# Optimization experiments

Hardware: AMD Instinct MI355X
Metric: run time of the kernel (lower is better)

The kernel has to match this reference:

```python
import jax, jax.numpy as jnp
import numpy as np

N = 200000
HID = 256
HEADS = 8
HD = HID // HEADS
C = 1000  # num clusters


def setup_inputs() -> dict:
    key = jax.random.key(0)
    ks = jax.random.split(key, 8)
    s = 1.0 / np.sqrt(HID)
    return {
        "x": jax.random.normal(ks[0], (N, HID), dtype=jnp.float32),
        "cluster_assignments": jax.random.randint(ks[1], (N,), 0, C),
        "batch": jnp.zeros((N,), dtype=jnp.int64),
        "Wk": jax.random.uniform(ks[2], (HID, HID), minval=-s, maxval=s),
        "bk": jnp.zeros((HID,), dtype=jnp.float32),
        "Wv": jax.random.uniform(ks[3], (HID, HID), minval=-s, maxval=s),
        "bv": jnp.zeros((HID,), dtype=jnp.float32),
        "Wo": jax.random.uniform(ks[4], (HID, HID), minval=-s, maxval=s),
        "bo": jnp.zeros((HID,), dtype=jnp.float32),
        "pool_query": jax.random.normal(ks[5], (1, HEADS, HD), dtype=jnp.float32),
    }


def reference(x, cluster_assignments, batch, Wk, bk, Wv, bv, Wo, bo, pool_query):
    seg = cluster_assignments
    scale = HD ** -0.5
    keys = (x @ Wk.T + bk).reshape(-1, HEADS, HD)     # [N, H, D]
    values = (x @ Wv.T + bv).reshape(-1, HEADS, HD)   # [N, H, D]
    # attention scores per node/head against shared pool query
    scores = jnp.einsum('nhd,hd->nh', keys, pool_query[0]) * scale  # [N, H]
    # segment-wise (per-cluster) softmax over nodes, per head
    m = jax.ops.segment_max(scores, seg, num_segments=C)            # [C, H]
    e = jnp.exp(scores - m[seg])                                    # [N, H]
    z = jax.ops.segment_sum(e, seg, num_segments=C)                 # [C, H]
    w = e / z[seg]                                                  # [N, H]
    attended = (w[..., None] * values).reshape(-1, HID)             # [N, HID]
    # scatter_mean over clusters
    ssum = jax.ops.segment_sum(attended, seg, num_segments=C)       # [C, HID]
    cnt = jax.ops.segment_sum(jnp.ones((attended.shape[0],), attended.dtype), seg, num_segments=C)
    pooled = ssum / jnp.clip(cnt, 1.0)[:, None]                     # [C, HID]
    out = pooled @ Wo.T + bo                                        # [C, HID]
    return out[seg]                                                 # [N, HID]
```

## Files before the change

kernel.cpp:

```cpp
#include <hip/hip_runtime.h>
#include <math.h>

#define HID 256
#define HEADS 8
#define HD 32
#define C_CLUST 1000
#define SCALEQ 0.17677669529663687f
#define CAP 512

__device__ inline unsigned enc_m(float f) {
  unsigned b = __float_as_uint(f);
  unsigned mask = (b & 0x80000000u) ? 0xFFFFFFFFu : 0x80000000u;
  return b ^ mask;
}
__device__ inline float dec_m(unsigned u) {
  unsigned b = (u & 0x80000000u) ? (u ^ 0x80000000u) : ~u;
  return __uint_as_float(b);
}

__global__ __launch_bounds__(256) void k_prep(const float* __restrict__ Wk,
                                              const float* __restrict__ bk,
                                              const float* __restrict__ pq,
                                              float* __restrict__ qk,
                                              float* __restrict__ cb,
                                              int* __restrict__ cur,
                                              unsigned* __restrict__ mtab) {
  __shared__ float qv[HD];
  int h = blockIdx.x;
  int t = threadIdx.x;
  int g = h * 256 + t;
  for (int i = g; i < C_CLUST; i += 2048) cur[i] = 0;
  for (int i = g; i < C_CLUST * 8; i += 2048) mtab[i] = 0u;
  if (t < HD) qv[t] = pq[h * HD + t];
  __syncthreads();
  float a = 0.f;
#pragma unroll 8
  for (int d = 0; d < HD; ++d) a += Wk[(size_t)(h * HD + d) * HID + t] * qv[d];
  qk[h * HID + t] = a * SCALEQ;
  if (t == 0) {
    float s = 0.f;
    for (int d = 0; d < HD; ++d) s += bk[h * HD + d] * qv[d];
    cb[h] = s * SCALEQ;
  }
}

__global__ __launch_bounds__(256) void k_scores(const float* __restrict__ x,
                                                const int* __restrict__ seg,
                                                const float* __restrict__ qk,
                                                const float* __restrict__ cb,
                                                float* __restrict__ scores,
                                                int* __restrict__ cur,
                                                unsigned* __restrict__ mtab,
                                                int* __restrict__ list, int N) {
  int lane = threadIdx.x & 63;
  int wid = (int)(((size_t)blockIdx.x * blockDim.x + threadIdx.x) >> 6);
  int nw = (int)(((size_t)gridDim.x * blockDim.x) >> 6);
  float4 q4[8];
#pragma unroll
  for (int h = 0; h < 8; ++h) q4[h] = *(const float4*)(qk + h * HID + 4 * lane);
  float cbv = cb[lane & 7];
  for (int n = wid; n < N; n += nw) {
    float4 xv = *(const float4*)(x + (size_t)n * HID + 4 * lane);
    float r0 = xv.x * q4[0].x + xv.y * q4[0].y + xv.z * q4[0].z + xv.w * q4[0].w;
    float r1 = xv.x * q4[1].x + xv.y * q4[1].y + xv.z * q4[1].z + xv.w * q4[1].w;
    float r2 = xv.x * q4[2].x + xv.y * q4[2].y + xv.z * q4[2].z + xv.w * q4[2].w;
    float r3 = xv.x * q4[3].x + xv.y * q4[3].y + xv.z * q4[3].z + xv.w * q4[3].w;
    float r4 = xv.x * q4[4].x + xv.y * q4[4].y + xv.z * q4[4].z + xv.w * q4[4].w;
    float r5 = xv.x * q4[5].x + xv.y * q4[5].y + xv.z * q4[5].z + xv.w * q4[5].w;
    float r6 = xv.x * q4[6].x + xv.y * q4[6].y + xv.z * q4[6].z + xv.w * q4[6].w;
    float r7 = xv.x * q4[7].x + xv.y * q4[7].y + xv.z * q4[7].z + xv.w * q4[7].w;
    r0 += __shfl_xor(r0, 1); r0 += __shfl_xor(r0, 2); r0 += __shfl_xor(r0, 4);
    r1 += __shfl_xor(r1, 1); r1 += __shfl_xor(r1, 2); r1 += __shfl_xor(r1, 4);
    r2 += __shfl_xor(r2, 1); r2 += __shfl_xor(r2, 2); r2 += __shfl_xor(r2, 4);
    r3 += __shfl_xor(r3, 1); r3 += __shfl_xor(r3, 2); r3 += __shfl_xor(r3, 4);
    r4 += __shfl_xor(r4, 1); r4 += __shfl_xor(r4, 2); r4 += __shfl_xor(r4, 4);
    r5 += __shfl_xor(r5, 1); r5 += __shfl_xor(r5, 2); r5 += __shfl_xor(r5, 4);
    r6 += __shfl_xor(r6, 1); r6 += __shfl_xor(r6, 2); r6 += __shfl_xor(r6, 4);
    r7 += __shfl_xor(r7, 1); r7 += __shfl_xor(r7, 2); r7 += __shfl_xor(r7, 4);
    int p = lane & 7;
    float v = (p < 4) ? ((p < 2) ? (p == 0 ? r0 : r1) : (p == 2 ? r2 : r3))
                      : ((p < 6) ? (p == 4 ? r4 : r5) : (p == 6 ? r6 : r7));
    v += __shfl_xor(v, 8); v += __shfl_xor(v, 16); v += __shfl_xor(v, 32);
    v += cbv;
    if (lane < 8) {
      int c = seg[n];
      scores[(size_t)n * 8 + lane] = v;
      atomicMax(&mtab[c * 8 + lane], enc_m(v));
      if (lane == 0) {
        int pos = atomicAdd(&cur[c], 1);
        if (pos < CAP) list[c * CAP + pos] = n;
      }
    }
  }
}

__global__ __launch_bounds__(256) void k_pool(const float* __restrict__ x,
                                              const float* __restrict__ scores,
                                              const unsigned* __restrict__ mtab,
                                              const int* __restrict__ cur,
                                              const int* __restrict__ list,
                                              const float* __restrict__ Wv,
                                              const float* __restrict__ bv,
                                              const float* __restrict__ Wo,
                                              const float* __restrict__ bo,
                                              float* __restrict__ outc) {
  __shared__ float e_lds[CAP][8];
  __shared__ float s_lds[8 * HID];
  __shared__ float red[256];
  __shared__ float p_lds[HID];
  int c = blockIdx.x;
  int t = threadIdx.x;
  int cnt = cur[c];
  if (cnt == 0) return;
  int cntL = (cnt < CAP) ? cnt : CAP;

  int h8 = t & 7;
  int i0 = t >> 3;
  int rq = t >> 6, cl = t & 63;
  float mh = dec_m(mtab[c * 8 + h8]);
  const int* lp = list + c * CAP;

  float pz = 0.f;
  for (int i = i0; i < cntL; i += 32) {
    float ev = __expf(scores[(size_t)lp[i] * 8 + h8] - mh);
    e_lds[i][h8] = ev;
    pz += ev;
  }
  red[t] = pz;
  __syncthreads();

  float4 acc[8];
#pragma unroll
  for (int h = 0; h < 8; ++h) acc[h] = make_float4(0.f, 0.f, 0.f, 0.f);
  int i = rq;
  for (; i + 12 < cntL; i += 16) {
    int n0 = lp[i], n1 = lp[i + 4], n2 = lp[i + 8], n3 = lp[i + 12];
    float4 x0 = *(const float4*)(x + (size_t)n0 * HID + 4 * cl);
    float4 x1 = *(const float4*)(x + (size_t)n1 * HID + 4 * cl);
    float4 x2 = *(const float4*)(x + (size_t)n2 * HID + 4 * cl);
    float4 x3 = *(const float4*)(x + (size_t)n3 * HID + 4 * cl);
    float4 ea, eb;
#define ACC8(XV, ROW)                                                        \
    ea = *(const float4*)&e_lds[ROW][0]; eb = *(const float4*)&e_lds[ROW][4]; \
    { float eh[8] = {ea.x, ea.y, ea.z, ea.w, eb.x, eb.y, eb.z, eb.w};         \
      _Pragma("unroll")                                                       \
      for (int h = 0; h < 8; ++h) {                                           \
        acc[h].x += eh[h] * XV.x; acc[h].y += eh[h] * XV.y;                   \
        acc[h].z += eh[h] * XV.z; acc[h].w += eh[h] * XV.w; } }
    ACC8(x0, i)
    ACC8(x1, i + 4)
    ACC8(x2, i + 8)
    ACC8(x3, i + 12)
  }
  for (; i < cntL; i += 4) {
    int n0 = lp[i];
    float4 x0 = *(const float4*)(x + (size_t)n0 * HID + 4 * cl);
    float4 ea, eb;
    ACC8(x0, i)
  }
#undef ACC8

  for (int s = 128; s >= 8; s >>= 1) {
    __syncthreads();
    if (t < s) red[t] += red[t + s];
  }
  __syncthreads();
  float zinv[8];
#pragma unroll
  for (int h = 0; h < 8; ++h) {
    float z = red[h];
    zinv[h] = (z > 0.f) ? 1.f / z : 0.f;
  }

  float4* buf = (float4*)e_lds;
#pragma unroll
  for (int h = 0; h < 8; ++h) {
    __syncthreads();
    buf[t] = acc[h];
    __syncthreads();
    if (t < 64) {
      float4 a = buf[t], b = buf[t + 64], c4 = buf[t + 128], d4 = buf[t + 192];
      float sc = zinv[h];
      float4 r;
      r.x = (a.x + b.x + c4.x + d4.x) * sc;
      r.y = (a.y + b.y + c4.y + d4.y) * sc;
      r.z = (a.z + b.z + c4.z + d4.z) * sc;
      r.w = (a.w + b.w + c4.w + d4.w) * sc;
      *(float4*)&s_lds[h * HID + 4 * t] = r;
    }
  }
  __syncthreads();

  int grp = t >> 2, q = t & 3;
  float rc = 1.f / (float)cnt;
#pragma unroll
  for (int r = 0; r < 4; ++r) {
    int o = grp + 64 * r;
    const float4* wr = (const float4*)(Wv + (size_t)o * HID);
    const float4* sr = (const float4*)(s_lds + (o >> 5) * HID);
    float a = 0.f;
#pragma unroll
    for (int k = 0; k < 16; ++k) {
      float4 w4 = wr[q + 4 * k];
      float4 s4 = sr[q + 4 * k];
      a += w4.x * s4.x + w4.y * s4.y + w4.z * s4.z + w4.w * s4.w;
    }
    a += __shfl_xor(a, 1);
    a += __shfl_xor(a, 2);
    if (q == 0) p_lds[o] = (a + bv[o]) * rc;
  }
  __syncthreads();
#pragma unroll
  for (int r = 0; r < 4; ++r) {
    int o = grp + 64 * r;
    const float4* wr = (const float4*)(Wo + (size_t)o * HID);
    const float4* pr = (const float4*)p_lds;
    float a = 0.f;
#pragma unroll
    for (int k = 0; k < 16; ++k) {
      float4 w4 = wr[q + 4 * k];
      float4 p4 = pr[q + 4 * k];
      a += w4.x * p4.x + w4.y * p4.y + w4.z * p4.z + w4.w * p4.w;
    }
    a += __shfl_xor(a, 1);
    a += __shfl_xor(a, 2);
    if (q == 0) outc[(size_t)c * HID + o] = a + bo[o];
  }
}

__global__ __launch_bounds__(256) void k_expand(const int* __restrict__ seg,
                                                const float* __restrict__ out_c,
                                                float* __restrict__ out, int N) {
  size_t g = (size_t)blockIdx.x * blockDim.x + threadIdx.x;
  size_t total = (size_t)N * (HID / 4);
  size_t stride = (size_t)gridDim.x * blockDim.x;
  const float4* oc = (const float4*)out_c;
  float4* o4 = (float4*)out;
  for (; g < total; g += stride) {
    int n = (int)(g >> 6);
    int q = (int)(g & 63);
    int c = seg[n];
    o4[g] = oc[(size_t)c * 64 + q];
  }
}

extern "C" void kernel_launch(void* const* d_in, const int* in_sizes, int n_in,
                              void* d_out, int out_size, void* d_ws, size_t ws_size,
                              hipStream_t stream) {
  const float* x = (const float*)d_in[0];
  const int* seg = (const int*)d_in[1];
  const float* Wk = (const float*)d_in[3];
  const float* bk = (const float*)d_in[4];
  const float* Wv = (const float*)d_in[5];
  const float* bv = (const float*)d_in[6];
  const float* Wo = (const float*)d_in[7];
  const float* bo = (const float*)d_in[8];
  const float* pq = (const float*)d_in[9];
  int N = in_sizes[0] / HID;

  char* ws = (char*)d_ws;
  size_t cur_off = 0;
  auto take = [&](size_t bytes) -> void* {
    void* p = ws + cur_off;
    cur_off += (bytes + 255) & ~(size_t)255;
    return p;
  };
  float* qk = (float*)take((size_t)HEADS * HID * 4);
  float* cb = (float*)take((size_t)HEADS * 4);
  int* cur = (int*)take((size_t)C_CLUST * 4);
  unsigned* mtab = (unsigned*)take((size_t)C_CLUST * 8 * 4);
  int* list = (int*)take((size_t)C_CLUST * CAP * 4);
  float* scr = (float*)take((size_t)N * 8 * 4);
  float* outc = (float*)take((size_t)C_CLUST * HID * 4);

  k_prep<<<HEADS, 256, 0, stream>>>(Wk, bk, pq, qk, cb, cur, mtab);
  int sb = (N + 31) / 32;
  k_scores<<<sb, 256, 0, stream>>>(x, seg, qk, cb, scr, cur, mtab, list, N);
  k_pool<<<C_CLUST, 256, 0, stream>>>(x, scr, mtab, cur, list, Wv, bv, Wo, bo, outc);
  k_expand<<<2048, 256, 0, stream>>>(seg, outc, (float*)d_out, N);
}
```

Measured before the change: 190.1 us.

## Fuse cluster-output expansion into pool kernel and deepen gather unroll

New measurement: 180.2 us. 1.05x faster.

```diff
diff --git a/kernel.cpp b/kernel.cpp
--- a/kernel.cpp
+++ b/kernel.cpp
@@ -7,6 +7,8 @@
 #define C_CLUST 1000
 #define SCALEQ 0.17677669529663687f
 #define CAP 512
+
+typedef float fx4 __attribute__((ext_vector_type(4)));
 
 __device__ inline unsigned enc_m(float f) {
   unsigned b = __float_as_uint(f);
@@ -103,11 +105,12 @@
                                               const float* __restrict__ bv,
                                               const float* __restrict__ Wo,
                                               const float* __restrict__ bo,
-                                              float* __restrict__ outc) {
+                                              float* __restrict__ out) {
   __shared__ float e_lds[CAP][8];
   __shared__ float s_lds[8 * HID];
   __shared__ float red[256];
   __shared__ float p_lds[HID];
+  __shared__ float orow[HID];
   int c = blockIdx.x;
   int t = threadIdx.x;
   int cnt = cur[c];
@@ -132,30 +135,33 @@
   float4 acc[8];
 #pragma unroll
   for (int h = 0; h < 8; ++h) acc[h] = make_float4(0.f, 0.f, 0.f, 0.f);
+  const float* xb = x + 4 * cl;
+#define ACC8(XV, ROW)                                                          \
+  { float4 ea = *(const float4*)&e_lds[ROW][0];                                \
+    float4 eb = *(const float4*)&e_lds[ROW][4];                                \
+    float eh[8] = {ea.x, ea.y, ea.z, ea.w, eb.x, eb.y, eb.z, eb.w};            \
+    _Pragma("unroll")                                                          \
+    for (int h = 0; h < 8; ++h) {                                              \
+      acc[h].x += eh[h] * XV.x; acc[h].y += eh[h] * XV.y;                      \
+      acc[h].z += eh[h] * XV.z; acc[h].w += eh[h] * XV.w; } }
   int i = rq;
-  for (; i + 12 < cntL; i += 16) {
-    int n0 = lp[i], n1 = lp[i + 4], n2 = lp[i + 8], n3 = lp[i + 12];
-    float4 x0 = *(const float4*)(x + (size_t)n0 * HID + 4 * cl);
-    float4 x1 = *(const float4*)(x + (size_t)n1 * HID + 4 * cl);
-    float4 x2 = *(const float4*)(x + (size_t)n2 * HID + 4 * cl);
-    float4 x3 = *(const float4*)(x + (size_t)n3 * HID + 4 * cl);
-    float4 ea, eb;
-#define ACC8(XV, ROW)                                                        \
-    ea = *(const float4*)&e_lds[ROW][0]; eb = *(const float4*)&e_lds[ROW][4]; \
-    { float eh[8] = {ea.x, ea.y, ea.z, ea.w, eb.x, eb.y, eb.z, eb.w};         \
-      _Pragma("unroll")                                                       \
-      for (int h = 0; h < 8; ++h) {                                           \
-        acc[h].x += eh[h] * XV.x; acc[h].y += eh[h] * XV.y;                   \
-        acc[h].z += eh[h] * XV.z; acc[h].w += eh[h] * XV.w; } }
-    ACC8(x0, i)
-    ACC8(x1, i + 4)
-    ACC8(x2, i + 8)
-    ACC8(x3, i + 12)
+  for (; i + 28 < cntL; i += 32) {
+    int n0 = lp[i +  0], n1 = lp[i +  4], n2 = lp[i +  8], n3 = lp[i + 12];
+    int n4 = lp[i + 16], n5 = lp[i + 20], n6 = lp[i + 24], n7 = lp[i + 28];
+    float4 x0 = *(const float4*)(xb + (size_t)n0 * HID);
+    float4 x1 = *(const float4*)(xb + (size_t)n1 * HID);
+    float4 x2 = *(const float4*)(xb + (size_t)n2 * HID);
+    float4 x3 = *(const float4*)(xb + (size_t)n3 * HID);
+    float4 x4 = *(const float4*)(xb + (size_t)n4 * HID);
+    float4 x5 = *(const float4*)(xb + (size_t)n5 * HID);
+    float4 x6 = *(const float4*)(xb + (size_t)n6 * HID);
+    float4 x7 = *(const float4*)(xb + (size_t)n7 * HID);
+    ACC8(x0, i +  0) ACC8(x1, i +  4) ACC8(x2, i +  8) ACC8(x3, i + 12)
+    ACC8(x4, i + 16) ACC8(x5, i + 20) ACC8(x6, i + 24) ACC8(x7, i + 28)
   }
   for (; i < cntL; i += 4) {
     int n0 = lp[i];
-    float4 x0 = *(const float4*)(x + (size_t)n0 * HID + 4 * cl);
-    float4 ea, eb;
+    float4 x0 = *(const float4*)(xb + (size_t)n0 * HID);
     ACC8(x0, i)
   }
 #undef ACC8
@@ -224,23 +230,14 @@
     }
     a += __shfl_xor(a, 1);
     a += __shfl_xor(a, 2);
-    if (q == 0) outc[(size_t)c * HID + o] = a + bo[o];
-  }
-}
-
-__global__ __launch_bounds__(256) void k_expand(const int* __restrict__ seg,
-                                                const float* __restrict__ out_c,
-                                                float* __restrict__ out, int N) {
-  size_t g = (size_t)blockIdx.x * blockDim.x + threadIdx.x;
-  size_t total = (size_t)N * (HID / 4);
-  size_t stride = (size_t)gridDim.x * blockDim.x;
-  const float4* oc = (const float4*)out_c;
-  float4* o4 = (float4*)out;
-  for (; g < total; g += stride) {
-    int n = (int)(g >> 6);
-    int q = (int)(g & 63);
-    int c = seg[n];
-    o4[g] = oc[(size_t)c * 64 + q];
+    if (q == 0) orow[o] = a + bo[o];
+  }
+  __syncthreads();
+
+  fx4 ov = *(const fx4*)&orow[4 * cl];
+  for (int j = rq; j < cnt; j += 4) {
+    int n = lp[j];
+    __builtin_nontemporal_store(ov, (fx4*)(out + (size_t)n * HID + 4 * cl));
   }
 }
 
@@ -271,11 +268,10 @@
   unsigned* mtab = (unsigned*)take((size_t)C_CLUST * 8 * 4);
   int* list = (int*)take((size_t)C_CLUST * CAP * 4);
   float* scr = (float*)take((size_t)N * 8 * 4);
-  float* outc = (float*)take((size_t)C_CLUST * HID * 4);
 
   k_prep<<<HEADS, 256, 0, stream>>>(Wk, bk, pq, qk, cb, cur, mtab);
   int sb = (N + 31) / 32;
   k_scores<<<sb, 256, 0, stream>>>(x, seg, qk, cb, scr, cur, mtab, list, N);
-  k_pool<<<C_CLUST, 256, 0, stream>>>(x, scr, mtab, cur, list, Wv, bv, Wo, bo, outc);
-  k_expand<<<2048, 256, 0, stream>>>(seg, outc, (float*)d_out, N);
-}
+  k_pool<<<C_CLUST, 256, 0, stream>>>(x, scr, mtab, cur, list, Wv, bv, Wo, bo,
+                                      (float*)d_out);
+}
```
